# Kernel tuning notes

Measured on AMD Instinct MI355X. Metric: run time of the kernel, lower is better.

## Reference

```python
import jax, jax.numpy as jnp
import numpy as np

N = 8192
F_IN = 512
F_OUT = 256
NEG_SLOPE = 0.01  # F.leaky_relu default
MASK_VAL = -1000000000000000.0


def setup_inputs() -> dict:
    key = jax.random.key(0)
    k1, k2, k3, k4 = jax.random.split(key, 4)
    stdv = 1.0 / np.sqrt(F_OUT)
    x = jax.random.normal(k1, (N, F_IN), dtype=jnp.float32)
    weight = jax.random.uniform(k2, (F_IN, F_OUT), dtype=jnp.float32, minval=-stdv, maxval=stdv)
    att_vec = jax.random.normal(k3, (2 * F_OUT, 1), dtype=jnp.float32) * 0.05
    adj = jax.random.randint(k4, (N, N), 0, 2, dtype=jnp.int32)
    return {"x": x, "weight": weight, "att_vec": att_vec, "adj": adj}


def _pair_indices(n):
    # Reproduces the (buggy-but-faithful) torch.cat(dim=0).view(n,-1,2f) indexing:
    # element (i,j,:f)  = out[idx(2m)], element (i,j,f:) = out[idx(2m+1)], m = i*n+j
    # idx(r) = r // n if r < n*n else (r - n*n) % n
    nn_ = n * n
    m = jnp.arange(nn_, dtype=jnp.int32)
    r0 = 2 * m
    r1 = r0 + 1
    idx1 = jnp.where(r0 < nn_, r0 // n, (r0 - nn_) % n)
    idx2 = jnp.where(r1 < nn_, r1 // n, (r1 - nn_) % n)
    return idx1, idx2


def reference(x, weight, att_vec, adj):
    n = x.shape[0]
    f = weight.shape[1]
    # dropout p=0.0 -> identity
    out = x @ weight                      # (n, f)
    a1 = att_vec[:f, 0]                   # (f,)
    a2 = att_vec[f:, 0]                   # (f,)
    s1 = out @ a1                         # (n,)
    s2 = out @ a2                         # (n,)
    idx1, idx2 = _pair_indices(n)
    scores = (s1[idx1] + s2[idx2]).reshape(n, n)
    scores = jax.nn.leaky_relu(scores, NEG_SLOPE)
    scores = jnp.where(adj > 0, scores, MASK_VAL)
    attn = jax.nn.softmax(scores, axis=1)  # F.softmax default dim=1 for 2D
    return jax.nn.sigmoid(attn @ out)      # (n, f)
```

## Files before the change

kernel.cpp:

```cpp
#include <hip/hip_runtime.h>

using u32 = unsigned int;
using u16 = unsigned short;

typedef __attribute__((ext_vector_type(8)))  __bf16 bf16x8;
typedef __attribute__((ext_vector_type(16))) float  f32x16;
typedef __attribute__((ext_vector_type(4)))  float  f32x4;
typedef __attribute__((ext_vector_type(4)))  int    i32x4;

__device__ __forceinline__ u32 f2bf(float f){
  u32 u = __float_as_uint(f);
  return (u + 0x7FFFu + ((u >> 16) & 1u)) >> 16;
}
__device__ __forceinline__ u32 pack2bf(float lo, float hi){
  return f2bf(lo) | (f2bf(hi) << 16);
}
__device__ __forceinline__ float bfu2f(u32 us){ return __uint_as_float(us << 16); }
__device__ __forceinline__ float lrelu(float x){ return x > 0.f ? x : 0.01f * x; }

__global__ void k0_wt(const float* __restrict__ w, u16* __restrict__ wT){
  int u = blockIdx.x * 256 + threadIdx.x;
  int k = u >> 8, n = u & 255;
  wT[(size_t)n * 512 + k] = (u16)f2bf(w[(size_t)k * 256 + n]);
}

__global__ __launch_bounds__(512, 2) void k1_gemm(const float* __restrict__ x,
    const u16* __restrict__ wT, const float* __restrict__ av, u16* __restrict__ outF,
    float* __restrict__ v0, float* __restrict__ v1, u16* __restrict__ pbf){
  __shared__ float tb[8][32][36];
  __shared__ float afl[512];
  __shared__ float sred[2][32][17];
  __shared__ float srw[2][32];
  const int i0 = blockIdx.x * 32;
  const int tid = threadIdx.x;
  const int lane = tid & 63, wv = tid >> 6;
  const int r = lane & 31, h = lane >> 5;
  const float* xp = x + (size_t)(i0 + r) * 512 + h * 8;
  const u16*   bp = wT + (size_t)(wv * 32 + r) * 512 + h * 8;
  f32x16 acc = {};
  for (int s = 0; s < 32; ++s){
    f32x4 a0 = *(const f32x4*)xp;
    f32x4 a1 = *(const f32x4*)(xp + 4);
    i32x4 pk = { (int)pack2bf(a0[0], a0[1]), (int)pack2bf(a0[2], a0[3]),
                 (int)pack2bf(a1[0], a1[1]), (int)pack2bf(a1[2], a1[3]) };
    bf16x8 af = __builtin_bit_cast(bf16x8, pk);
    bf16x8 bf = *(const bf16x8*)bp;
    acc = __builtin_amdgcn_mfma_f32_32x32x16_bf16(af, bf, acc, 0, 0, 0);
    xp += 16; bp += 16;
  }
  #pragma unroll
  for (int re = 0; re < 16; ++re){
    int rr = (re & 3) + 8 * (re >> 2) + 4 * h;
    tb[wv][r][rr] = acc[re];
  }
  afl[tid] = av[tid];
  __syncthreads();
  {
    const int n2 = lane >> 1, ic = (lane & 1) * 16;
    const float* tp = &tb[wv][n2][ic];
    i32x4 w0 = { (int)pack2bf(tp[0],tp[1]),   (int)pack2bf(tp[2],tp[3]),
                 (int)pack2bf(tp[4],tp[5]),   (int)pack2bf(tp[6],tp[7]) };
    i32x4 w1 = { (int)pack2bf(tp[8],tp[9]),   (int)pack2bf(tp[10],tp[11]),
                 (int)pack2bf(tp[12],tp[13]), (int)pack2bf(tp[14],tp[15]) };
    const int n = wv * 32 + n2;
    const int k16 = (i0 + ic) >> 4;
    u16* op = outF + ((size_t)k16 * 256 + n) * 16;
    *(i32x4*)op = w0;
    *((i32x4*)op + 1) = w1;
  }
  const int row = tid & 31, g = tid >> 5;
  const int w8 = g >> 1, fh = (g & 1) * 16;
  float a1c = 0.f, a2c = 0.f;
  #pragma unroll
  for (int f = 0; f < 16; ++f){
    float tv = tb[w8][fh + f][row];
    a1c = fmaf(tv, afl[w8 * 32 + fh + f], a1c);
    a2c = fmaf(tv, afl[256 + w8 * 32 + fh + f], a2c);
  }
  sred[0][row][g] = a1c; sred[1][row][g] = a2c;
  __syncthreads();
  if (tid < 64){
    int which = tid >> 5, r2 = tid & 31;
    float s = 0.f;
    #pragma unroll
    for (int g2 = 0; g2 < 16; ++g2) s += sred[which][r2][g2];
    srw[which][r2] = s;
  }
  __syncthreads();
  if (tid < 16){
    int k = (i0 >> 1) + tid;
    float sa  = srw[0][2*tid],   sb  = srw[1][2*tid];
    float sa1 = srw[0][2*tid+1], sb1 = srw[1][2*tid+1];
    v0[k] = lrelu(sa + sb);
    v1[k] = lrelu(sa1 + sb1);
    float w = lrelu(sa + sb1);
    pbf[k] = (u16)f2bf(__expf(w));
  }
}

__global__ __launch_bounds__(512, 1) void k3_main(const int* __restrict__ adj,
    const u16* __restrict__ outF, const u16* __restrict__ pbf,
    float* __restrict__ P, float* __restrict__ pd){
  __shared__ u16 AbS[2][16768];
  __shared__ u32 plS[2048];
  const int bid = blockIdx.x;
  const int xcd = bid & 7, grp = bid >> 3;
  const int half = xcd & 1, c = (xcd >> 1) & 1, hi = xcd >> 2;
  const int tile = half * 64 + hi * 32 + grp;
  const bool top = (half == 0);
  const int i0 = tile * 64;
  const int kbase = c * 4096;
  const int pb = tile * 2 + c;
  const int tid = threadIdx.x, l = tid & 63, w = tid >> 6;
  const int r = l & 31, h = l >> 5;
  const bool isProd = (w < 4);
  const int w4 = w & 3;

  if (top){
    plS[tid] = 0x3F803F80u;        plS[tid + 512] = 0x3F803F80u;
    plS[tid + 1024] = 0x3F803F80u; plS[tid + 1536] = 0x3F803F80u;
  } else {
    const u32* ps = (const u32*)pbf;
    plS[tid] = ps[tid];             plS[tid + 512] = ps[tid + 512];
    plS[tid + 1024] = ps[tid + 1024]; plS[tid + 1536] = ps[tid + 1536];
  }
  __syncthreads();

  const int* aq0 = adj + (size_t)(i0 + w4 * 16) * 8192 + kbase + l * 4;
  u16* const wp0 = &AbS[0][0] + (l >> 2) * 1048 + ((l >> 1) & 1) * 512
                   + 4 * (l & 1) + w4 * 128;
  const int fb = w4 * 64;
  const u16* bq0 = outF + (size_t)c * 1048576 + (fb + r) * 16 + h * 8;

  i32x4 ar[16];
  float dd[16] = {0.f,0.f,0.f,0.f,0.f,0.f,0.f,0.f,0.f,0.f,0.f,0.f,0.f,0.f,0.f,0.f};
  bf16x8 BA[8], BB[8];
  f32x16 a00 = {}, a01 = {}, a10 = {}, a11 = {};

#define ISSUE(T_) { _Pragma("unroll") for (int j_ = 0; j_ < 16; ++j_) \
    ar[j_] = *(const i32x4*)(aq0 + (size_t)j_ * 8192 + (T_) * 256); \
  asm volatile("" ::: "memory"); }

#define BFS(W_) (__uint_as_float((W_) << 16) + __uint_as_float((W_) & 0xFFFF0000u))

#define PACKALL(T_,BUF_) { \
  u32 pp0_ = plS[(T_) * 128 + 2 * l]; \
  u32 pp1_ = plS[(T_) * 128 + 2 * l + 1]; \
  u16* wb_ = wp0 + (BUF_) * 16768; \
  _Pragma("unroll") for (int j_ = 0; j_ < 16; ++j_){ \
    i32x4 a_ = ar[j_]; \
    u32 w0_ = ((((u32)(-a_[0])) & 0xFFFFu) | (((u32)(-a_[1])) << 16)) & pp0_; \
    u32 w1_ = ((((u32)(-a_[2])) & 0xFFFFu) | (((u32)(-a_[3])) << 16)) & pp1_; \
    dd[j_] += BFS(w0_) + BFS(w1_); \
    uint2 wv_; wv_.x = w0_; wv_.y = w1_; \
    *(uint2*)(wb_ + j_ * 8) = wv_; } }

#define B_ISS(B_,G_) { const u16* bb_ = bq0 + (size_t)(G_) * 4096; \
  _Pragma("unroll") for (int j_ = 0; j_ < 4; ++j_){ \
    B_[2*j_]   = *(const bf16x8*)(bb_ + j_ * 4096); \
    B_[2*j_+1] = *(const bf16x8*)(bb_ + j_ * 4096 + 512); } \
  asm volatile("" ::: "memory"); }

#define MFMA4(B_,BUF_,S0_) { \
  const u16* rb_ = &AbS[0][0] + (BUF_) * 16768 + (S0_) * 1048 + h * 512 + r * 8; \
  __builtin_amdgcn_s_setprio(1); \
  _Pragma("unroll") for (int j_ = 0; j_ < 4; ++j_){ \
    bf16x8 a0_ = *(const bf16x8*)(rb_ + j_ * 1048); \
    bf16x8 a1_ = *(const bf16x8*)(rb_ + j_ * 1048 + 256); \
    a00 = __builtin_amdgcn_mfma_f32_32x32x16_bf16(a0_, B_[2*j_],   a00, 0, 0, 0); \
    a01 = __builtin_amdgcn_mfma_f32_32x32x16_bf16(a0_, B_[2*j_+1], a01, 0, 0, 0); \
    a10 = __builtin_amdgcn_mfma_f32_32x32x16_bf16(a1_, B_[2*j_],   a10, 0, 0, 0); \
    a11 = __builtin_amdgcn_mfma_f32_32x32x16_bf16(a1_, B_[2*j_+1], a11, 0, 0, 0); } \
  __builtin_amdgcn_s_setprio(0); }

#define KBAR() { asm volatile("s_waitcnt lgkmcnt(0)" ::: "memory"); \
  __builtin_amdgcn_s_barrier(); asm volatile("" ::: "memory"); }

  if (isProd){ ISSUE(0); } else { B_ISS(BA, 0); }
  #pragma unroll 1
  for (int t = 0; t <= 16; ++t){
    if (isProd){
      if (t < 16){
        PACKALL(t, t & 1);
        if (t < 15) ISSUE(t + 1);
      }
    } else {
      if (t >= 1){
        const int ph = t - 1, buf = ph & 1, g0 = ph * 16;
        B_ISS(BB, g0 + 4);  MFMA4(BA, buf, 0);
        B_ISS(BA, g0 + 8);  MFMA4(BB, buf, 4);
        B_ISS(BB, g0 + 12); MFMA4(BA, buf, 8);
        if (ph < 15){ B_ISS(BA, g0 + 16); }
        MFMA4(BB, buf, 12);
      }
    }
    KBAR();
  }

#undef ISSUE
#undef PACKALL
#undef B_ISS
#undef MFMA4
#undef KBAR
#undef BFS

  if (isProd){
    #pragma unroll
    for (int j = 0; j < 16; ++j){
      float v = dd[j];
      #pragma unroll
      for (int mk = 1; mk < 64; mk <<= 1) v += __shfl_xor(v, mk);
      if (l == 0) pd[(size_t)pb * 64 + w4 * 16 + j] = v;
    }
  } else {
    float* Pb = P + (size_t)pb * 16384 + fb + r;
    #pragma unroll
    for (int e = 0; e < 16; ++e){
      int rr = (e & 3) + 8 * (e >> 2) + 4 * h;
      __builtin_nontemporal_store(a00[e], Pb + (size_t)rr * 256);
      __builtin_nontemporal_store(a01[e], Pb + (size_t)rr * 256 + 32);
      __builtin_nontemporal_store(a10[e], Pb + (size_t)(rr + 32) * 256);
      __builtin_nontemporal_store(a11[e], Pb + (size_t)(rr + 32) * 256 + 32);
    }
  }
}

__global__ void k4_final(const float* __restrict__ P, const float* __restrict__ pd,
    const float* __restrict__ v0, const float* __restrict__ v1, float* __restrict__ out){
  const int i = blockIdx.x, n = threadIdx.x;
  const int tile = i >> 6, rloc = i & 63;
  const size_t base = (size_t)(tile * 2) * 16384 + (size_t)rloc * 256 + n;
  float P0 = __builtin_nontemporal_load(P + base);
  float P1 = __builtin_nontemporal_load(P + base + 16384);
  float d0 = pd[tile * 128 + rloc];
  float d1 = pd[tile * 128 + 64 + rloc];
  float val;
  if (i < 4096){
    float va = v0[i], vb = v1[i];
    float m = fmaxf(va, vb);
    float e0 = __expf(va - m), e1 = __expf(vb - m);
    val = (e0 * P0 + e1 * P1) / (e0 * d0 + e1 * d1);
  } else {
    val = (P0 + P1) / (d0 + d1);
  }
  out[(size_t)i * 256 + n] = 1.0f / (1.0f + __expf(-val));
}

extern "C" void kernel_launch(void* const* d_in, const int* in_sizes, int n_in,
                              void* d_out, int out_size, void* d_ws, size_t ws_size,
                              hipStream_t stream)
{
  const float* x      = (const float*)d_in[0];
  const float* weight = (const float*)d_in[1];
  const float* av     = (const float*)d_in[2];
  const int*   adj    = (const int*)d_in[3];
  float* out = (float*)d_out;
  char* ws = (char*)d_ws;
  float* P     = (float*)(ws + 0);
  float* pd    = (float*)(ws + 16777216);
  u16*   outF  = (u16*)  (ws + 16842752);
  u16*   wT    = (u16*)  (ws + 21037056);
  u16*   pbf   = (u16*)  (ws + 21299200);
  float* v0    = (float*)(ws + 21307392);
  float* v1    = (float*)(ws + 21323776);

  k0_wt   <<<512, 256, 0, stream>>>(weight, wT);
  k1_gemm <<<256, 512, 0, stream>>>(x, wT, av, outF, v0, v1, pbf);
  k3_main <<<256, 512, 0, stream>>>(adj, outF, pbf, P, pd);
  k4_final<<<8192, 256, 0, stream>>>(P, pd, v0, v1, out);
}
```

Measured before the change: 105.3 us.

## Fuse final softmax-normalize and sigmoid into main kernel, drop split-K partials

Drops the split-K scheme, in which two blocks each handled half of K for a 64-row tile and wrote fp32 partials that a fourth kernel combined. Each block now covers 32 rows over the full K range with 1024 threads: 8 producer waves pack the adjacency tiles and 8 MFMA waves compute a 32-column slice each. Normalization and the sigmoid move into the epilogue, so the P/pd round trip through memory and the k4 launch go away. The two per-row softmax weights are precomputed in bf16 in k1, which adds some rounding. Each block now runs a longer serial K loop (32 steps) with fewer blocks in parallel per tile.

```diff
diff --git a/kernel.cpp b/kernel.cpp
--- a/kernel.cpp
+++ b/kernel.cpp
@@ -26,7 +26,7 @@
 
 __global__ __launch_bounds__(512, 2) void k1_gemm(const float* __restrict__ x,
     const u16* __restrict__ wT, const float* __restrict__ av, u16* __restrict__ outF,
-    float* __restrict__ v0, float* __restrict__ v1, u16* __restrict__ pbf){
+    u32* __restrict__ etp, u16* __restrict__ pbf){
   __shared__ float tb[8][32][36];
   __shared__ float afl[512];
   __shared__ float sred[2][32][17];
@@ -91,159 +91,145 @@
     int k = (i0 >> 1) + tid;
     float sa  = srw[0][2*tid],   sb  = srw[1][2*tid];
     float sa1 = srw[0][2*tid+1], sb1 = srw[1][2*tid+1];
-    v0[k] = lrelu(sa + sb);
-    v1[k] = lrelu(sa1 + sb1);
+    float va = lrelu(sa + sb);
+    float vb = lrelu(sa1 + sb1);
+    float m = fmaxf(va, vb);
+    etp[k] = pack2bf(__expf(va - m), __expf(vb - m));
     float w = lrelu(sa + sb1);
     pbf[k] = (u16)f2bf(__expf(w));
   }
 }
 
-__global__ __launch_bounds__(512, 1) void k3_main(const int* __restrict__ adj,
+__global__ __launch_bounds__(1024, 1) void k3_main(const int* __restrict__ adj,
     const u16* __restrict__ outF, const u16* __restrict__ pbf,
-    float* __restrict__ P, float* __restrict__ pd){
-  __shared__ u16 AbS[2][16768];
+    const u32* __restrict__ etp, float* __restrict__ out){
+  __shared__ u16 AbS[2][8448];
   __shared__ u32 plS[2048];
-  const int bid = blockIdx.x;
-  const int xcd = bid & 7, grp = bid >> 3;
-  const int half = xcd & 1, c = (xcd >> 1) & 1, hi = xcd >> 2;
-  const int tile = half * 64 + hi * 32 + grp;
-  const bool top = (half == 0);
-  const int i0 = tile * 64;
-  const int kbase = c * 4096;
-  const int pb = tile * 2 + c;
+  __shared__ u32 etS[32];
+  __shared__ float dS[32];
+  const int tile = blockIdx.x;
+  const bool top = tile < 128;
+  const int i0 = tile * 32;
   const int tid = threadIdx.x, l = tid & 63, w = tid >> 6;
   const int r = l & 31, h = l >> 5;
-  const bool isProd = (w < 4);
-  const int w4 = w & 3;
+  const bool isProd = (w < 8);
+  const int w8 = w & 7;
 
   if (top){
-    plS[tid] = 0x3F803F80u;        plS[tid + 512] = 0x3F803F80u;
-    plS[tid + 1024] = 0x3F803F80u; plS[tid + 1536] = 0x3F803F80u;
+    if (tid < 32) etS[tid] = etp[i0 + tid];
   } else {
     const u32* ps = (const u32*)pbf;
-    plS[tid] = ps[tid];             plS[tid + 512] = ps[tid + 512];
-    plS[tid + 1024] = ps[tid + 1024]; plS[tid + 1536] = ps[tid + 1536];
-  }
-  __syncthreads();
-
-  const int* aq0 = adj + (size_t)(i0 + w4 * 16) * 8192 + kbase + l * 4;
-  u16* const wp0 = &AbS[0][0] + (l >> 2) * 1048 + ((l >> 1) & 1) * 512
-                   + 4 * (l & 1) + w4 * 128;
-  const int fb = w4 * 64;
-  const u16* bq0 = outF + (size_t)c * 1048576 + (fb + r) * 16 + h * 8;
-
-  i32x4 ar[16];
-  float dd[16] = {0.f,0.f,0.f,0.f,0.f,0.f,0.f,0.f,0.f,0.f,0.f,0.f,0.f,0.f,0.f,0.f};
-  bf16x8 BA[8], BB[8];
-  f32x16 a00 = {}, a01 = {}, a10 = {}, a11 = {};
-
-#define ISSUE(T_) { _Pragma("unroll") for (int j_ = 0; j_ < 16; ++j_) \
-    ar[j_] = *(const i32x4*)(aq0 + (size_t)j_ * 8192 + (T_) * 256); \
+    plS[tid] = ps[tid];
+    plS[tid + 1024] = ps[tid + 1024];
+  }
+  __syncthreads();
+
+  const int* aq0 = adj + (size_t)(i0 + w8 * 4) * 8192 + l * 4;
+  u16* const wp0 = &AbS[0][0] + (l >> 2) * 528 + ((l >> 1) & 1) * 256
+                   + 4 * (l & 1) + w8 * 32;
+  const int fb = w8 * 32;
+  const u16* bq0 = outF + (size_t)(fb + r) * 16 + h * 8;
+
+  i32x4 arA[4], arB[4];
+  float dd[4] = {0.f, 0.f, 0.f, 0.f};
+  bf16x8 BA[4], BB[4];
+  f32x16 acc = {};
+
+#define ISSUE(AR_,T_) { _Pragma("unroll") for (int j_ = 0; j_ < 4; ++j_) \
+    AR_[j_] = __builtin_nontemporal_load((const i32x4*)(aq0 + (size_t)j_ * 8192 + (T_) * 256)); \
   asm volatile("" ::: "memory"); }
 
 #define BFS(W_) (__uint_as_float((W_) << 16) + __uint_as_float((W_) & 0xFFFF0000u))
 
-#define PACKALL(T_,BUF_) { \
-  u32 pp0_ = plS[(T_) * 128 + 2 * l]; \
-  u32 pp1_ = plS[(T_) * 128 + 2 * l + 1]; \
-  u16* wb_ = wp0 + (BUF_) * 16768; \
-  _Pragma("unroll") for (int j_ = 0; j_ < 16; ++j_){ \
-    i32x4 a_ = ar[j_]; \
-    u32 w0_ = ((((u32)(-a_[0])) & 0xFFFFu) | (((u32)(-a_[1])) << 16)) & pp0_; \
-    u32 w1_ = ((((u32)(-a_[2])) & 0xFFFFu) | (((u32)(-a_[3])) << 16)) & pp1_; \
+#define PACK(AR_,T_,BUF_) { \
+  u32 c0_ = 0, c1_ = 0; \
+  if (!top){ c0_ = plS[((T_) & 15) * 128 + 2 * l]; \
+             c1_ = plS[((T_) & 15) * 128 + 2 * l + 1]; } \
+  u16* wb_ = wp0 + (BUF_) * 8448; \
+  _Pragma("unroll") for (int j_ = 0; j_ < 4; ++j_){ \
+    i32x4 a_ = AR_[j_]; \
+    u32 m0_ = (((u32)(-a_[0])) & 0xFFFFu) | (((u32)(-a_[1])) << 16); \
+    u32 m1_ = (((u32)(-a_[2])) & 0xFFFFu) | (((u32)(-a_[3])) << 16); \
+    u32 p0_, p1_; \
+    if (top){ u32 ep_ = etS[w8 * 4 + j_]; \
+              u32 e_ = ((T_) >= 16) ? (ep_ >> 16) : (ep_ & 0xFFFFu); \
+              p0_ = e_ | (e_ << 16); p1_ = p0_; } \
+    else { p0_ = c0_; p1_ = c1_; } \
+    u32 w0_ = m0_ & p0_, w1_ = m1_ & p1_; \
     dd[j_] += BFS(w0_) + BFS(w1_); \
     uint2 wv_; wv_.x = w0_; wv_.y = w1_; \
     *(uint2*)(wb_ + j_ * 8) = wv_; } }
 
 #define B_ISS(B_,G_) { const u16* bb_ = bq0 + (size_t)(G_) * 4096; \
-  _Pragma("unroll") for (int j_ = 0; j_ < 4; ++j_){ \
-    B_[2*j_]   = *(const bf16x8*)(bb_ + j_ * 4096); \
-    B_[2*j_+1] = *(const bf16x8*)(bb_ + j_ * 4096 + 512); } \
+  _Pragma("unroll") for (int j_ = 0; j_ < 4; ++j_) \
+    B_[j_] = *(const bf16x8*)(bb_ + j_ * 4096); \
   asm volatile("" ::: "memory"); }
 
 #define MFMA4(B_,BUF_,S0_) { \
-  const u16* rb_ = &AbS[0][0] + (BUF_) * 16768 + (S0_) * 1048 + h * 512 + r * 8; \
+  const u16* rb_ = &AbS[0][0] + (BUF_) * 8448 + (S0_) * 528 + h * 256 + r * 8; \
   __builtin_amdgcn_s_setprio(1); \
   _Pragma("unroll") for (int j_ = 0; j_ < 4; ++j_){ \
-    bf16x8 a0_ = *(const bf16x8*)(rb_ + j_ * 1048); \
-    bf16x8 a1_ = *(const bf16x8*)(rb_ + j_ * 1048 + 256); \
-    a00 = __builtin_amdgcn_mfma_f32_32x32x16_bf16(a0_, B_[2*j_],   a00, 0, 0, 0); \
-    a01 = __builtin_amdgcn_mfma_f32_32x32x16_bf16(a0_, B_[2*j_+1], a01, 0, 0, 0); \
-    a10 = __builtin_amdgcn_mfma_f32_32x32x16_bf16(a1_, B_[2*j_],   a10, 0, 0, 0); \
-    a11 = __builtin_amdgcn_mfma_f32_32x32x16_bf16(a1_, B_[2*j_+1], a11, 0, 0, 0); } \
+    bf16x8 a_ = *(const bf16x8*)(rb_ + j_ * 528); \
+    acc = __builtin_amdgcn_mfma_f32_32x32x16_bf16(a_, B_[j_], acc, 0, 0, 0); } \
   __builtin_amdgcn_s_setprio(0); }
 
 #define KBAR() { asm volatile("s_waitcnt lgkmcnt(0)" ::: "memory"); \
   __builtin_amdgcn_s_barrier(); asm volatile("" ::: "memory"); }
 
-  if (isProd){ ISSUE(0); } else { B_ISS(BA, 0); }
+  if (isProd){ ISSUE(arA, 0); } else { B_ISS(BA, 0); }
   #pragma unroll 1
-  for (int t = 0; t <= 16; ++t){
+  for (int t = 0; t < 32; ++t){
     if (isProd){
-      if (t < 16){
-        PACKALL(t, t & 1);
-        if (t < 15) ISSUE(t + 1);
+      if (t & 1){
+        if (t < 31) ISSUE(arA, t + 1);
+        PACK(arB, t, t & 1);
+      } else {
+        if (t < 31) ISSUE(arB, t + 1);
+        PACK(arA, t, t & 1);
       }
-    } else {
-      if (t >= 1){
-        const int ph = t - 1, buf = ph & 1, g0 = ph * 16;
-        B_ISS(BB, g0 + 4);  MFMA4(BA, buf, 0);
-        B_ISS(BA, g0 + 8);  MFMA4(BB, buf, 4);
-        B_ISS(BB, g0 + 12); MFMA4(BA, buf, 8);
-        if (ph < 15){ B_ISS(BA, g0 + 16); }
-        MFMA4(BB, buf, 12);
-      }
+    } else if (t >= 1){
+      const int ph = t - 1, buf = ph & 1, g0 = ph * 16;
+      B_ISS(BB, g0 + 4);  MFMA4(BA, buf, 0);
+      B_ISS(BA, g0 + 8);  MFMA4(BB, buf, 4);
+      B_ISS(BB, g0 + 12); MFMA4(BA, buf, 8);
+      B_ISS(BA, g0 + 16); MFMA4(BB, buf, 12);
     }
     KBAR();
   }
+  if (isProd){
+    #pragma unroll
+    for (int j = 0; j < 4; ++j){
+      float v = dd[j];
+      #pragma unroll
+      for (int mk = 1; mk < 64; mk <<= 1) v += __shfl_xor(v, mk);
+      if (l == 0) dS[w8 * 4 + j] = v;
+    }
+  } else {
+    const int buf = 1, g0 = 496;
+    B_ISS(BB, g0 + 4);  MFMA4(BA, buf, 0);
+    B_ISS(BA, g0 + 8);  MFMA4(BB, buf, 4);
+    B_ISS(BB, g0 + 12); MFMA4(BA, buf, 8);
+    MFMA4(BB, buf, 12);
+  }
+  KBAR();
 
 #undef ISSUE
-#undef PACKALL
+#undef PACK
 #undef B_ISS
 #undef MFMA4
 #undef KBAR
 #undef BFS
 
-  if (isProd){
-    #pragma unroll
-    for (int j = 0; j < 16; ++j){
-      float v = dd[j];
-      #pragma unroll
-      for (int mk = 1; mk < 64; mk <<= 1) v += __shfl_xor(v, mk);
-      if (l == 0) pd[(size_t)pb * 64 + w4 * 16 + j] = v;
-    }
-  } else {
-    float* Pb = P + (size_t)pb * 16384 + fb + r;
+  if (!isProd){
+    float* ob = out + (size_t)i0 * 256 + fb + (l & 31);
     #pragma unroll
     for (int e = 0; e < 16; ++e){
       int rr = (e & 3) + 8 * (e >> 2) + 4 * h;
-      __builtin_nontemporal_store(a00[e], Pb + (size_t)rr * 256);
-      __builtin_nontemporal_store(a01[e], Pb + (size_t)rr * 256 + 32);
-      __builtin_nontemporal_store(a10[e], Pb + (size_t)(rr + 32) * 256);
-      __builtin_nontemporal_store(a11[e], Pb + (size_t)(rr + 32) * 256 + 32);
+      float val = acc[e] / dS[rr];
+      float sg = 1.0f / (1.0f + __expf(-val));
+      __builtin_nontemporal_store(sg, ob + (size_t)rr * 256);
     }
   }
-}
-
-__global__ void k4_final(const float* __restrict__ P, const float* __restrict__ pd,
-    const float* __restrict__ v0, const float* __restrict__ v1, float* __restrict__ out){
-  const int i = blockIdx.x, n = threadIdx.x;
-  const int tile = i >> 6, rloc = i & 63;
-  const size_t base = (size_t)(tile * 2) * 16384 + (size_t)rloc * 256 + n;
-  float P0 = __builtin_nontemporal_load(P + base);
-  float P1 = __builtin_nontemporal_load(P + base + 16384);
-  float d0 = pd[tile * 128 + rloc];
-  float d1 = pd[tile * 128 + 64 + rloc];
-  float val;
-  if (i < 4096){
-    float va = v0[i], vb = v1[i];
-    float m = fmaxf(va, vb);
-    float e0 = __expf(va - m), e1 = __expf(vb - m);
-    val = (e0 * P0 + e1 * P1) / (e0 * d0 + e1 * d1);
-  } else {
-    val = (P0 + P1) / (d0 + d1);
-  }
-  out[(size_t)i * 256 + n] = 1.0f / (1.0f + __expf(-val));
 }
 
 extern "C" void kernel_launch(void* const* d_in, const int* in_sizes, int n_in,
@@ -256,16 +242,12 @@
   const int*   adj    = (const int*)d_in[3];
   float* out = (float*)d_out;
   char* ws = (char*)d_ws;
-  float* P     = (float*)(ws + 0);
-  float* pd    = (float*)(ws + 16777216);
-  u16*   outF  = (u16*)  (ws + 16842752);
-  u16*   wT    = (u16*)  (ws + 21037056);
-  u16*   pbf   = (u16*)  (ws + 21299200);
-  float* v0    = (float*)(ws + 21307392);
-  float* v1    = (float*)(ws + 21323776);
+  u16*   outF  = (u16*)(ws + 0);
+  u16*   wT    = (u16*)(ws + 4194304);
+  u16*   pbf   = (u16*)(ws + 4456448);
+  u32*   etp   = (u32*)(ws + 4464640);
 
   k0_wt   <<<512, 256, 0, stream>>>(weight, wT);
-  k1_gemm <<<256, 512, 0, stream>>>(x, wT, av, outF, v0, v1, pbf);
-  k3_main <<<256, 512, 0, stream>>>(adj, outF, pbf, P, pd);
-  k4_final<<<8192, 256, 0, stream>>>(P, pd, v0, v1, out);
-}
+  k1_gemm <<<256, 512, 0, stream>>>(x, wT, av, outF, etp, pbf);
+  k3_main <<<256, 1024, 0, stream>>>(adj, outF, pbf, etp, out);
+}
```

Measured after the change: 124.0 us. +17.8%, slower.
